# Optimization experiments

Hardware: AMD Instinct MI355X
Metric: run time of the kernel (lower is better)

Reference implementation:

```python
import jax, jax.numpy as jnp
import numpy as np

NEG_INF = -1e30
LRELU_SLOPE = 0.01
KEEP_SCALE = 2.0  # 1/(1-p) with p=0.5


def mixed_act(x, tid):
    # x: [B, H], tid: [H] int type ids
    # 0 relu, 1 tanh, 2 sig, 3 'smin'->Softmax, 4 'smax'->Softmin, 5 gelu, 6 lrelu
    relu = jnp.maximum(x, 0.0)
    tanh = jnp.tanh(x)
    sig = jax.nn.sigmoid(x)
    gelu = jax.nn.gelu(x, approximate=False)
    lrelu = jnp.where(x >= 0, x, LRELU_SLOPE * x)
    # softmax/softmin restricted to the columns of that type (matches x[:, idx] gather)
    smin = jax.nn.softmax(jnp.where(tid == 3, x, NEG_INF), axis=1)
    smax = jax.nn.softmax(jnp.where(tid == 4, -x, NEG_INF), axis=1)
    return jnp.select(
        [tid == 0, tid == 1, tid == 2, tid == 3, tid == 4, tid == 5, tid == 6],
        [relu, tanh, sig, smin, smax, gelu, lrelu],
    )


def setup_inputs() -> dict:
    key = jax.random.key(0)
    ks = jax.random.split(key, 16)
    B, D_IN, H, C = 32768, 784, 1024, 10
    s_in, s_h = 1.0 / np.sqrt(D_IN), 1.0 / np.sqrt(H)
    inp = {
        "x": jax.random.normal(ks[0], (B, D_IN), jnp.float32),
        "W0": jax.random.normal(ks[1], (H, D_IN), jnp.float32) * s_in,
        "b0": jax.random.normal(ks[2], (H,), jnp.float32) * s_in,
        "W1": jax.random.normal(ks[3], (H, H), jnp.float32) * s_h,
        "b1": jax.random.normal(ks[4], (H,), jnp.float32) * s_h,
        "W2": jax.random.normal(ks[5], (H, H), jnp.float32) * s_h,
        "b2": jax.random.normal(ks[6], (H,), jnp.float32) * s_h,
        "W3": jax.random.normal(ks[7], (C, H), jnp.float32) * s_h,
        "b3": jax.random.normal(ks[8], (C,), jnp.float32) * s_h,
        "mask1": jax.random.bernoulli(ks[9], 0.5, (B, H)).astype(jnp.float32),
        "mask2": jax.random.bernoulli(ks[10], 0.5, (B, H)).astype(jnp.float32),
        "mask3": jax.random.bernoulli(ks[11], 0.5, (B, H)).astype(jnp.float32),
        "type_ids": jax.random.randint(ks[12], (3, H), 0, 7, jnp.int32),
    }
    return inp


def reference(x, W0, b0, W1, b1, W2, b2, W3, b3, mask1, mask2, mask3, type_ids):
    h = mixed_act(x @ W0.T + b0, type_ids[0])
    h = mixed_act((h * mask1 * KEEP_SCALE) @ W1.T + b1, type_ids[1])
    h = mixed_act((h * mask2 * KEEP_SCALE) @ W2.T + b2, type_ids[2])
    logits = (h * mask3 * KEEP_SCALE) @ W3.T + b3
    out = jax.nn.log_softmax(logits, axis=1)
    return (out, mask1, mask2, mask3)
```

## Files before the change

### kernel.cpp

```cpp
#include <hip/hip_runtime.h>
#include <hip/hip_bf16.h>
#include <cstdint>
#include <cstddef>

typedef __bf16 bf16_t;
typedef bf16_t bf16x8 __attribute__((ext_vector_type(8)));
typedef bf16_t bf16x4 __attribute__((ext_vector_type(4)));
typedef float f32x4 __attribute__((ext_vector_type(4)));

#define NEG_BIG (-1e30f)

__global__ __launch_bounds__(256) void convert_pad(const float* __restrict__ src,
                                                   bf16_t* __restrict__ dst,
                                                   int incols, int outcols) {
    const int row = blockIdx.x;
    const float* s = src + (size_t)row * incols;
    bf16_t* d = dst + (size_t)row * outcols;
    const int n4 = outcols >> 2;
    for (int c = threadIdx.x; c < n4; c += blockDim.x) {
        const int col = c << 2;
        float4 v;
        if (col < incols) v = *(const float4*)(s + col);
        else              v = make_float4(0.f, 0.f, 0.f, 0.f);
        bf16x4 o;
        o[0] = (bf16_t)v.x; o[1] = (bf16_t)v.y; o[2] = (bf16_t)v.z; o[3] = (bf16_t)v.w;
        *(bf16x4*)(d + col) = o;
    }
}

#define BM 128
#define BN 128
#define BK 32

__global__ __launch_bounds__(256) void gemm_bt(const bf16_t* __restrict__ A,
                                               const bf16_t* __restrict__ W,
                                               const float* __restrict__ bias,
                                               bf16_t* __restrict__ Z,
                                               int K, int N) {
    __shared__ __align__(16) bf16_t As[BM * BK];
    __shared__ __align__(16) bf16_t Bs[BN * BK];
    const int tid  = threadIdx.x;
    const int wid  = tid >> 6;
    const int lane = tid & 63;
    const int n0 = blockIdx.x * BN;
    const int m0 = blockIdx.y * BM;

    const int wm = (wid >> 1) * 64;
    const int wn = (wid & 1) * 64;

    f32x4 acc[4][4] = {};

    const int srow0 = wid * 32 + (lane >> 2);
    const int scol  = (lane & 3) * 8;

    const bf16_t* Aptr0 = A + (size_t)(m0 + srow0) * K + scol;
    const bf16_t* Aptr1 = A + (size_t)(m0 + srow0 + 16) * K + scol;
    const bf16_t* Wptr0 = W + (size_t)(n0 + srow0) * K + scol;
    const bf16_t* Wptr1 = W + (size_t)(n0 + srow0 + 16) * K + scol;

    bf16_t* AsB0 = As + (wid * 2 + 0) * 512;
    bf16_t* AsB1 = As + (wid * 2 + 1) * 512;
    bf16_t* BsB0 = Bs + (wid * 2 + 0) * 512;
    bf16_t* BsB1 = Bs + (wid * 2 + 1) * 512;

    for (int k0 = 0; k0 < K; k0 += BK) {
        __syncthreads();
        __builtin_amdgcn_global_load_lds((const __attribute__((address_space(1))) void*)(Aptr0 + k0),
                                         (__attribute__((address_space(3))) void*)AsB0, 16, 0, 0);
        __builtin_amdgcn_global_load_lds((const __attribute__((address_space(1))) void*)(Aptr1 + k0),
                                         (__attribute__((address_space(3))) void*)AsB1, 16, 0, 0);
        __builtin_amdgcn_global_load_lds((const __attribute__((address_space(1))) void*)(Wptr0 + k0),
                                         (__attribute__((address_space(3))) void*)BsB0, 16, 0, 0);
        __builtin_amdgcn_global_load_lds((const __attribute__((address_space(1))) void*)(Wptr1 + k0),
                                         (__attribute__((address_space(3))) void*)BsB1, 16, 0, 0);
        __syncthreads();

        const int arow = wm + (lane & 15);
        const int brow = wn + (lane & 15);
        const int koff = (lane >> 4) * 8;
        bf16x8 af[4], bfr[4];
        #pragma unroll
        for (int i = 0; i < 4; ++i)
            af[i] = *(const bf16x8*)(As + (arow + i * 16) * BK + koff);
        #pragma unroll
        for (int j = 0; j < 4; ++j)
            bfr[j] = *(const bf16x8*)(Bs + (brow + j * 16) * BK + koff);
        #pragma unroll
        for (int i = 0; i < 4; ++i)
            #pragma unroll
            for (int j = 0; j < 4; ++j)
                acc[i][j] = __builtin_amdgcn_mfma_f32_16x16x32_bf16(af[i], bfr[j], acc[i][j], 0, 0, 0);
    }

    const int cq = lane >> 4;
    const int cl = lane & 15;
    #pragma unroll
    for (int j = 0; j < 4; ++j) {
        const int col = n0 + wn + j * 16 + cl;
        const float bj = bias[col];
        #pragma unroll
        for (int i = 0; i < 4; ++i) {
            const int row = m0 + wm + i * 16 + cq * 4;
            #pragma unroll
            for (int r = 0; r < 4; ++r)
                Z[(size_t)(row + r) * N + col] = (bf16_t)(acc[i][j][r] + bj);
        }
    }
}

__global__ __launch_bounds__(256) void act_kernel(const bf16_t* __restrict__ Z,
                                                  const float* __restrict__ mask,
                                                  const int* __restrict__ tids,
                                                  bf16_t* __restrict__ H,
                                                  float* __restrict__ mask_out) {
    const int row  = blockIdx.x;
    const int t    = threadIdx.x;
    const int wid  = t >> 6;
    const int lane = t & 63;
    __shared__ float r3[4], r4[4];
    __shared__ float bc[4];

    const size_t base = (size_t)row * 1024 + t * 4;
    bf16x4 z4 = *(const bf16x4*)(Z + base);
    float z[4];
    #pragma unroll
    for (int j = 0; j < 4; ++j) z[j] = (float)z4[j];
    const int4 ty4 = *(const int4*)(tids + t * 4);
    const int ty[4] = {ty4.x, ty4.y, ty4.z, ty4.w};
    const float4 m4 = *(const float4*)(mask + base);
    const float mk[4] = {m4.x, m4.y, m4.z, m4.w};

    float mx3 = NEG_BIG, mx4 = NEG_BIG;
    #pragma unroll
    for (int j = 0; j < 4; ++j) {
        if (ty[j] == 3) mx3 = fmaxf(mx3, z[j]);
        if (ty[j] == 4) mx4 = fmaxf(mx4, -z[j]);
    }
    #pragma unroll
    for (int off = 32; off > 0; off >>= 1) {
        mx3 = fmaxf(mx3, __shfl_down(mx3, off));
        mx4 = fmaxf(mx4, __shfl_down(mx4, off));
    }
    if (lane == 0) { r3[wid] = mx3; r4[wid] = mx4; }
    __syncthreads();
    if (t == 0) {
        bc[0] = fmaxf(fmaxf(r3[0], r3[1]), fmaxf(r3[2], r3[3]));
        bc[1] = fmaxf(fmaxf(r4[0], r4[1]), fmaxf(r4[2], r4[3]));
    }
    __syncthreads();
    mx3 = bc[0]; mx4 = bc[1];

    float s3 = 0.f, s4 = 0.f;
    #pragma unroll
    for (int j = 0; j < 4; ++j) {
        if (ty[j] == 3) s3 += __expf(z[j] - mx3);
        if (ty[j] == 4) s4 += __expf(-z[j] - mx4);
    }
    #pragma unroll
    for (int off = 32; off > 0; off >>= 1) {
        s3 += __shfl_down(s3, off);
        s4 += __shfl_down(s4, off);
    }
    if (lane == 0) { r3[wid] = s3; r4[wid] = s4; }
    __syncthreads();
    if (t == 0) {
        bc[2] = r3[0] + r3[1] + r3[2] + r3[3];
        bc[3] = r4[0] + r4[1] + r4[2] + r4[3];
    }
    __syncthreads();
    const float inv3 = 1.f / bc[2];
    const float inv4 = 1.f / bc[3];

    bf16x4 h4;
    #pragma unroll
    for (int j = 0; j < 4; ++j) {
        const float zz = z[j];
        const int tt = ty[j];
        float a;
        if (tt == 0)      a = fmaxf(zz, 0.f);
        else if (tt == 1) { const float e = __expf(-2.f * fabsf(zz));
                            const float th = (1.f - e) / (1.f + e);
                            a = (zz >= 0.f) ? th : -th; }
        else if (tt == 2) a = 1.f / (1.f + __expf(-zz));
        else if (tt == 3) a = __expf(zz - mx3) * inv3;
        else if (tt == 4) a = __expf(-zz - mx4) * inv4;
        else if (tt == 5) a = 0.5f * zz * (1.f + erff(zz * 0.70710678118654752f));
        else              a = (zz >= 0.f) ? zz : 0.01f * zz;
        h4[j] = (bf16_t)(a * mk[j] * 2.0f);
    }
    *(bf16x4*)(H + base) = h4;
    *(float4*)(mask_out + base) = m4;
}

__global__ __launch_bounds__(256) void final_layer(const bf16_t* __restrict__ H,
                                                   const float* __restrict__ W3,
                                                   const float* __restrict__ b3,
                                                   float* __restrict__ out) {
    __shared__ __align__(16) bf16_t Ws[10 * 1024];
    for (int i = threadIdx.x; i < 10240; i += 256) Ws[i] = (bf16_t)W3[i];
    __syncthreads();
    const int wid  = threadIdx.x >> 6;
    const int lane = threadIdx.x & 63;
    #pragma unroll 1
    for (int rr = 0; rr < 4; ++rr) {
        const int row = blockIdx.x * 16 + wid * 4 + rr;
        const bf16_t* hrow = H + (size_t)row * 1024;
        float acc[10];
        #pragma unroll
        for (int n = 0; n < 10; ++n) acc[n] = 0.f;
        #pragma unroll
        for (int c = 0; c < 2; ++c) {
            const int k = c * 512 + lane * 8;
            const bf16x8 hv = *(const bf16x8*)(hrow + k);
            float hf[8];
            #pragma unroll
            for (int j = 0; j < 8; ++j) hf[j] = (float)hv[j];
            #pragma unroll
            for (int n = 0; n < 10; ++n) {
                const bf16x8 wv = *(const bf16x8*)(Ws + n * 1024 + k);
                #pragma unroll
                for (int j = 0; j < 8; ++j) acc[n] += hf[j] * (float)wv[j];
            }
        }
        #pragma unroll
        for (int n = 0; n < 10; ++n)
            #pragma unroll
            for (int off = 32; off > 0; off >>= 1)
                acc[n] += __shfl_down(acc[n], off);
        if (lane == 0) {
            float lg[10]; float mx = -1e30f;
            #pragma unroll
            for (int n = 0; n < 10; ++n) { lg[n] = acc[n] + b3[n]; mx = fmaxf(mx, lg[n]); }
            float se = 0.f;
            #pragma unroll
            for (int n = 0; n < 10; ++n) se += __expf(lg[n] - mx);
            const float lse = logf(se) + mx;
            #pragma unroll
            for (int n = 0; n < 10; ++n) out[(size_t)row * 10 + n] = lg[n] - lse;
        }
    }
}

extern "C" void kernel_launch(void* const* d_in, const int* in_sizes, int n_in,
                              void* d_out, int out_size, void* d_ws, size_t ws_size,
                              hipStream_t stream) {
    (void)in_sizes; (void)n_in; (void)out_size; (void)ws_size;
    const float* x     = (const float*)d_in[0];
    const float* W0    = (const float*)d_in[1];
    const float* b0    = (const float*)d_in[2];
    const float* W1    = (const float*)d_in[3];
    const float* b1    = (const float*)d_in[4];
    const float* W2    = (const float*)d_in[5];
    const float* b2    = (const float*)d_in[6];
    const float* W3    = (const float*)d_in[7];
    const float* b3    = (const float*)d_in[8];
    const float* mask1 = (const float*)d_in[9];
    const float* mask2 = (const float*)d_in[10];
    const float* mask3 = (const float*)d_in[11];
    const int*   tids  = (const int*)d_in[12];

    float* out = (float*)d_out;
    float* mo1 = out + 327680;
    float* mo2 = mo1 + 33554432;
    float* mo3 = mo2 + 33554432;

    char* ws = (char*)d_ws;
    bf16_t* xb  = (bf16_t*)ws;  ws += (size_t)32768 * 800 * 2;
    bf16_t* W0b = (bf16_t*)ws;  ws += (size_t)1024 * 800 * 2;
    bf16_t* W1b = (bf16_t*)ws;  ws += (size_t)1024 * 1024 * 2;
    bf16_t* W2b = (bf16_t*)ws;  ws += (size_t)1024 * 1024 * 2;
    bf16_t* Zb  = (bf16_t*)ws;  ws += (size_t)32768 * 1024 * 2;
    bf16_t* hb  = (bf16_t*)ws;  ws += (size_t)32768 * 1024 * 2;

    convert_pad<<<32768, 256, 0, stream>>>(x,  xb,  784, 800);
    convert_pad<<<1024,  256, 0, stream>>>(W0, W0b, 784, 800);
    convert_pad<<<1024,  256, 0, stream>>>(W1, W1b, 1024, 1024);
    convert_pad<<<1024,  256, 0, stream>>>(W2, W2b, 1024, 1024);

    dim3 g(1024 / BN, 32768 / BM);
    gemm_bt<<<g, 256, 0, stream>>>(xb, W0b, b0, Zb, 800, 1024);
    act_kernel<<<32768, 256, 0, stream>>>(Zb, mask1, tids, hb, mo1);
    gemm_bt<<<g, 256, 0, stream>>>(hb, W1b, b1, Zb, 1024, 1024);
    act_kernel<<<32768, 256, 0, stream>>>(Zb, mask2, tids + 1024, hb, mo2);
    gemm_bt<<<g, 256, 0, stream>>>(hb, W2b, b2, Zb, 1024, 1024);
    act_kernel<<<32768, 256, 0, stream>>>(Zb, mask3, tids + 2048, hb, mo3);
    final_layer<<<2048, 256, 0, stream>>>(hb, W3, b3, out);
}
```

Before: 1.177 ms.

## Swizzle GEMM blocks across XCDs, one-wave-per-row activation, fuse last activation into output layer

The GEMM launch becomes a 1D grid, and block IDs are remapped so that consecutive tiles sharing operands land on the same XCD, which should improve L2 reuse. The activation kernel now processes one row per wave with a shuffle-only reduction, so shared memory and block barriers are gone. It also drops the max subtraction from the softmax terms and computes a single exp per element that is shared across tanh, sigmoid and softmax. The third activation is fused with the final 10-class projection and log-softmax, removing one bf16 write and re-read of the hidden matrix. Skipping the max subtraction risks overflow if pre-activations grow large.

```diff
diff --git a/kernel.cpp b/kernel.cpp
--- a/kernel.cpp
+++ b/kernel.cpp
@@ -42,8 +42,13 @@
     const int tid  = threadIdx.x;
     const int wid  = tid >> 6;
     const int lane = tid & 63;
-    const int n0 = blockIdx.x * BN;
-    const int m0 = blockIdx.y * BM;
+
+    const int bid = (int)blockIdx.x;
+    const int cpx = (int)gridDim.x >> 3;
+    const int swz = (bid & 7) * cpx + (bid >> 3);
+    const int nbn = N >> 7;
+    const int n0 = (swz % nbn) * BN;
+    const int m0 = (swz / nbn) * BM;
 
     const int wm = (wid >> 1) * 64;
     const int wn = (wid & 1) * 64;
@@ -113,120 +118,181 @@
                                                   const int* __restrict__ tids,
                                                   bf16_t* __restrict__ H,
                                                   float* __restrict__ mask_out) {
-    const int row  = blockIdx.x;
-    const int t    = threadIdx.x;
-    const int wid  = t >> 6;
-    const int lane = t & 63;
-    __shared__ float r3[4], r4[4];
-    __shared__ float bc[4];
-
-    const size_t base = (size_t)row * 1024 + t * 4;
-    bf16x4 z4 = *(const bf16x4*)(Z + base);
-    float z[4];
-    #pragma unroll
-    for (int j = 0; j < 4; ++j) z[j] = (float)z4[j];
-    const int4 ty4 = *(const int4*)(tids + t * 4);
-    const int ty[4] = {ty4.x, ty4.y, ty4.z, ty4.w};
-    const float4 m4 = *(const float4*)(mask + base);
-    const float mk[4] = {m4.x, m4.y, m4.z, m4.w};
-
-    float mx3 = NEG_BIG, mx4 = NEG_BIG;
-    #pragma unroll
-    for (int j = 0; j < 4; ++j) {
-        if (ty[j] == 3) mx3 = fmaxf(mx3, z[j]);
-        if (ty[j] == 4) mx4 = fmaxf(mx4, -z[j]);
-    }
-    #pragma unroll
-    for (int off = 32; off > 0; off >>= 1) {
-        mx3 = fmaxf(mx3, __shfl_down(mx3, off));
-        mx4 = fmaxf(mx4, __shfl_down(mx4, off));
-    }
-    if (lane == 0) { r3[wid] = mx3; r4[wid] = mx4; }
-    __syncthreads();
-    if (t == 0) {
-        bc[0] = fmaxf(fmaxf(r3[0], r3[1]), fmaxf(r3[2], r3[3]));
-        bc[1] = fmaxf(fmaxf(r4[0], r4[1]), fmaxf(r4[2], r4[3]));
-    }
-    __syncthreads();
-    mx3 = bc[0]; mx4 = bc[1];
-
-    float s3 = 0.f, s4 = 0.f;
-    #pragma unroll
-    for (int j = 0; j < 4; ++j) {
-        if (ty[j] == 3) s3 += __expf(z[j] - mx3);
-        if (ty[j] == 4) s4 += __expf(-z[j] - mx4);
-    }
-    #pragma unroll
-    for (int off = 32; off > 0; off >>= 1) {
-        s3 += __shfl_down(s3, off);
-        s4 += __shfl_down(s4, off);
-    }
-    if (lane == 0) { r3[wid] = s3; r4[wid] = s4; }
-    __syncthreads();
-    if (t == 0) {
-        bc[2] = r3[0] + r3[1] + r3[2] + r3[3];
-        bc[3] = r4[0] + r4[1] + r4[2] + r4[3];
-    }
-    __syncthreads();
-    const float inv3 = 1.f / bc[2];
-    const float inv4 = 1.f / bc[3];
-
-    bf16x4 h4;
-    #pragma unroll
-    for (int j = 0; j < 4; ++j) {
-        const float zz = z[j];
-        const int tt = ty[j];
-        float a;
-        if (tt == 0)      a = fmaxf(zz, 0.f);
-        else if (tt == 1) { const float e = __expf(-2.f * fabsf(zz));
-                            const float th = (1.f - e) / (1.f + e);
-                            a = (zz >= 0.f) ? th : -th; }
-        else if (tt == 2) a = 1.f / (1.f + __expf(-zz));
-        else if (tt == 3) a = __expf(zz - mx3) * inv3;
-        else if (tt == 4) a = __expf(-zz - mx4) * inv4;
-        else if (tt == 5) a = 0.5f * zz * (1.f + erff(zz * 0.70710678118654752f));
-        else              a = (zz >= 0.f) ? zz : 0.01f * zz;
-        h4[j] = (bf16_t)(a * mk[j] * 2.0f);
-    }
-    *(bf16x4*)(H + base) = h4;
-    *(float4*)(mask_out + base) = m4;
-}
-
-__global__ __launch_bounds__(256) void final_layer(const bf16_t* __restrict__ H,
-                                                   const float* __restrict__ W3,
-                                                   const float* __restrict__ b3,
-                                                   float* __restrict__ out) {
-    __shared__ __align__(16) bf16_t Ws[10 * 1024];
-    for (int i = threadIdx.x; i < 10240; i += 256) Ws[i] = (bf16_t)W3[i];
-    __syncthreads();
     const int wid  = threadIdx.x >> 6;
     const int lane = threadIdx.x & 63;
+    const int row  = (int)blockIdx.x * 4 + wid;
+    const size_t rb = (size_t)row * 1024;
+
+    float z[16], e[16];
+    int   ty[16];
+    float4 mk[4];
+    float s3 = 0.f, s4 = 0.f;
+
+    #pragma unroll
+    for (int q = 0; q < 4; ++q) {
+        const int c0 = (q * 64 + lane) * 4;
+        const bf16x4 z4 = *(const bf16x4*)(Z + rb + c0);
+        const int4   t4 = *(const int4*)(tids + c0);
+        mk[q] = *(const float4*)(mask + rb + c0);
+        const int tt[4] = {t4.x, t4.y, t4.z, t4.w};
+        #pragma unroll
+        for (int j = 0; j < 4; ++j) {
+            const int i = q * 4 + j;
+            const float zz = (float)z4[j];
+            z[i] = zz; ty[i] = tt[j];
+            const float az = fabsf(zz);
+            const float arg = (tt[j] == 1) ? -2.f * az
+                            : (tt[j] == 2) ? -az
+                            : (tt[j] == 3) ? zz
+                            : (tt[j] == 4) ? -zz : 0.f;
+            const float ee = __expf(arg);
+            e[i] = ee;
+            s3 += (tt[j] == 3) ? ee : 0.f;
+            s4 += (tt[j] == 4) ? ee : 0.f;
+        }
+    }
+    #pragma unroll
+    for (int off = 32; off > 0; off >>= 1) {
+        s3 += __shfl_xor(s3, off);
+        s4 += __shfl_xor(s4, off);
+    }
+    const float inv3 = 1.f / s3;
+    const float inv4 = 1.f / s4;
+
+    #pragma unroll
+    for (int q = 0; q < 4; ++q) {
+        const int c0 = (q * 64 + lane) * 4;
+        const float mm[4] = {mk[q].x, mk[q].y, mk[q].z, mk[q].w};
+        bf16x4 h4;
+        #pragma unroll
+        for (int j = 0; j < 4; ++j) {
+            const int i = q * 4 + j;
+            const float zz = z[i], ee = e[i];
+            const int tt = ty[i];
+            const float r1pe = __builtin_amdgcn_rcpf(1.f + ee);
+            const float tha = (1.f - ee) * r1pe;
+            const float tnh = (zz >= 0.f) ? tha : -tha;
+            const float sg  = ((zz >= 0.f) ? 1.f : ee) * r1pe;
+            const float gel = 0.5f * zz * (1.f + erff(zz * 0.70710678f));
+            const float a = (tt == 0) ? fmaxf(zz, 0.f)
+                          : (tt == 1) ? tnh
+                          : (tt == 2) ? sg
+                          : (tt == 3) ? ee * inv3
+                          : (tt == 4) ? ee * inv4
+                          : (tt == 5) ? gel
+                          : fmaxf(zz, 0.01f * zz);
+            h4[j] = (bf16_t)(a * mm[j] * 2.0f);
+        }
+        *(bf16x4*)(H + rb + c0) = h4;
+        *(float4*)(mask_out + rb + c0) = mk[q];
+    }
+}
+
+__global__ __launch_bounds__(256) void act_final(const bf16_t* __restrict__ Z,
+                                                 const float* __restrict__ mask,
+                                                 const int* __restrict__ tids,
+                                                 const float* __restrict__ W3,
+                                                 const float* __restrict__ b3,
+                                                 float* __restrict__ mask_out,
+                                                 float* __restrict__ out) {
+    __shared__ float Ws[10 * 1024];
+    for (int i = threadIdx.x; i < 10240; i += 256) Ws[i] = W3[i];
+    __syncthreads();
+
+    const int wid  = threadIdx.x >> 6;
+    const int lane = threadIdx.x & 63;
+
+    int ty[16];
+    #pragma unroll
+    for (int q = 0; q < 4; ++q) {
+        const int4 t4 = *(const int4*)(tids + (q * 64 + lane) * 4);
+        ty[q * 4 + 0] = t4.x; ty[q * 4 + 1] = t4.y;
+        ty[q * 4 + 2] = t4.z; ty[q * 4 + 3] = t4.w;
+    }
+
     #pragma unroll 1
     for (int rr = 0; rr < 4; ++rr) {
-        const int row = blockIdx.x * 16 + wid * 4 + rr;
-        const bf16_t* hrow = H + (size_t)row * 1024;
+        const int row = (int)blockIdx.x * 16 + wid * 4 + rr;
+        const size_t rb = (size_t)row * 1024;
+
+        float z[16], e[16], h[16];
+        float4 mk[4];
+        float s3 = 0.f, s4 = 0.f;
+
+        #pragma unroll
+        for (int q = 0; q < 4; ++q) {
+            const int c0 = (q * 64 + lane) * 4;
+            const bf16x4 z4 = *(const bf16x4*)(Z + rb + c0);
+            mk[q] = *(const float4*)(mask + rb + c0);
+            #pragma unroll
+            for (int j = 0; j < 4; ++j) {
+                const int i = q * 4 + j;
+                const float zz = (float)z4[j];
+                z[i] = zz;
+                const int tt = ty[i];
+                const float az = fabsf(zz);
+                const float arg = (tt == 1) ? -2.f * az
+                                : (tt == 2) ? -az
+                                : (tt == 3) ? zz
+                                : (tt == 4) ? -zz : 0.f;
+                const float ee = __expf(arg);
+                e[i] = ee;
+                s3 += (tt == 3) ? ee : 0.f;
+                s4 += (tt == 4) ? ee : 0.f;
+            }
+        }
+        #pragma unroll
+        for (int off = 32; off > 0; off >>= 1) {
+            s3 += __shfl_xor(s3, off);
+            s4 += __shfl_xor(s4, off);
+        }
+        const float inv3 = 1.f / s3;
+        const float inv4 = 1.f / s4;
+
+        #pragma unroll
+        for (int q = 0; q < 4; ++q) {
+            const int c0 = (q * 64 + lane) * 4;
+            const float mm[4] = {mk[q].x, mk[q].y, mk[q].z, mk[q].w};
+            #pragma unroll
+            for (int j = 0; j < 4; ++j) {
+                const int i = q * 4 + j;
+                const float zz = z[i], ee = e[i];
+                const int tt = ty[i];
+                const float r1pe = __builtin_amdgcn_rcpf(1.f + ee);
+                const float tha = (1.f - ee) * r1pe;
+                const float tnh = (zz >= 0.f) ? tha : -tha;
+                const float sg  = ((zz >= 0.f) ? 1.f : ee) * r1pe;
+                const float gel = 0.5f * zz * (1.f + erff(zz * 0.70710678f));
+                const float a = (tt == 0) ? fmaxf(zz, 0.f)
+                              : (tt == 1) ? tnh
+                              : (tt == 2) ? sg
+                              : (tt == 3) ? ee * inv3
+                              : (tt == 4) ? ee * inv4
+                              : (tt == 5) ? gel
+                              : fmaxf(zz, 0.01f * zz);
+                h[i] = a * mm[j] * 2.0f;
+            }
+            *(float4*)(mask_out + rb + c0) = mk[q];
+        }
+
         float acc[10];
         #pragma unroll
         for (int n = 0; n < 10; ++n) acc[n] = 0.f;
         #pragma unroll
-        for (int c = 0; c < 2; ++c) {
-            const int k = c * 512 + lane * 8;
-            const bf16x8 hv = *(const bf16x8*)(hrow + k);
-            float hf[8];
-            #pragma unroll
-            for (int j = 0; j < 8; ++j) hf[j] = (float)hv[j];
+        for (int q = 0; q < 4; ++q) {
+            const int c0 = (q * 64 + lane) * 4;
             #pragma unroll
             for (int n = 0; n < 10; ++n) {
-                const bf16x8 wv = *(const bf16x8*)(Ws + n * 1024 + k);
-                #pragma unroll
-                for (int j = 0; j < 8; ++j) acc[n] += hf[j] * (float)wv[j];
+                const float4 w = *(const float4*)(Ws + n * 1024 + c0);
+                acc[n] += h[q*4+0] * w.x + h[q*4+1] * w.y + h[q*4+2] * w.z + h[q*4+3] * w.w;
             }
         }
         #pragma unroll
         for (int n = 0; n < 10; ++n)
             #pragma unroll
             for (int off = 32; off > 0; off >>= 1)
-                acc[n] += __shfl_down(acc[n], off);
+                acc[n] += __shfl_xor(acc[n], off);
+
         if (lane == 0) {
             float lg[10]; float mx = -1e30f;
             #pragma unroll
@@ -277,12 +343,10 @@
     convert_pad<<<1024,  256, 0, stream>>>(W1, W1b, 1024, 1024);
     convert_pad<<<1024,  256, 0, stream>>>(W2, W2b, 1024, 1024);
 
-    dim3 g(1024 / BN, 32768 / BM);
-    gemm_bt<<<g, 256, 0, stream>>>(xb, W0b, b0, Zb, 800, 1024);
-    act_kernel<<<32768, 256, 0, stream>>>(Zb, mask1, tids, hb, mo1);
-    gemm_bt<<<g, 256, 0, stream>>>(hb, W1b, b1, Zb, 1024, 1024);
-    act_kernel<<<32768, 256, 0, stream>>>(Zb, mask2, tids + 1024, hb, mo2);
-    gemm_bt<<<g, 256, 0, stream>>>(hb, W2b, b2, Zb, 1024, 1024);
-    act_kernel<<<32768, 256, 0, stream>>>(Zb, mask3, tids + 2048, hb, mo3);
-    final_layer<<<2048, 256, 0, stream>>>(hb, W3, b3, out);
-}
+    gemm_bt<<<2048, 256, 0, stream>>>(xb, W0b, b0, Zb, 800, 1024);
+    act_kernel<<<8192, 256, 0, stream>>>(Zb, mask1, tids, hb, mo1);
+    gemm_bt<<<2048, 256, 0, stream>>>(hb, W1b, b1, Zb, 1024, 1024);
+    act_kernel<<<8192, 256, 0, stream>>>(Zb, mask2, tids + 1024, hb, mo2);
+    gemm_bt<<<2048, 256, 0, stream>>>(hb, W2b, b2, Zb, 1024, 1024);
+    act_final<<<2048, 256, 0, stream>>>(Zb, mask3, tids + 2048, W3, b3, mo3, out);
+}
```

Result: slower. 1.391 ms (+18.1%).
